# Performance work log

Hardware: AMD Instinct MI355X
Metric: run time of the kernel (lower is better)

Reference implementation:

```python
import jax, jax.numpy as jnp
import numpy as np

IN_FEATURES = 4096
OUT_FEATURES = 4096
BATCH, SEQ = 4, 2048

def setup_inputs() -> dict:
    key = jax.random.key(0)
    k1, k2, k3, k4, k5 = jax.random.split(key, 5)
    x = jax.random.normal(k1, (BATCH, SEQ, IN_FEATURES), dtype=jnp.float32)
    # int8 codes stored as int32 in [0, 255] (asymmetric uint8-style quantization)
    qweight = jax.random.randint(k2, (OUT_FEATURES, IN_FEATURES), 0, 255, dtype=jnp.int32)
    scales = jax.random.uniform(k3, (OUT_FEATURES,), dtype=jnp.float32) * 0.01 + 1e-3
    zero_points = jax.random.uniform(k4, (OUT_FEATURES,), dtype=jnp.float32) * 255.0
    bias = jax.random.normal(k5, (OUT_FEATURES,), dtype=jnp.float32)
    return {"x": x, "qweight": qweight, "scales": scales, "zero_points": zero_points, "bias": bias}

def reference(x, qweight, scales, zero_points, bias):
    # Per-output-channel dequantization: W[o, i] = (q[o, i] - zp[o]) * scale[o]
    w = (qweight.astype(jnp.float32) - zero_points[:, None]) * scales[:, None]  # [O, I]
    # y = x @ W.T + b, fused dequant + GEMM in the original ipex op
    y = jnp.einsum("bsi,oi->bso", x, w) + bias
    return y
```

## Files before the change

### kernel.cpp

```cpp
#include <hip/hip_runtime.h>
#include <hip/hip_bf16.h>

typedef __attribute__((ext_vector_type(4))) int i32x4;
typedef __attribute__((ext_vector_type(16))) int i32x16;

#define M_DIM 8192
#define N_DIM 4096
#define K_DIM 4096
#define BM 256
#define BN 256
#define BK 128
#define NT2 (K_DIM / BK)

static __device__ inline void gload_lds16(const void* g, void* l) {
  __builtin_amdgcn_global_load_lds(
      (const __attribute__((address_space(1))) unsigned int*)g,
      (__attribute__((address_space(3))) unsigned int*)l,
      16, 0, 0);
}

__global__ __launch_bounds__(256) void prep_x_i8(
    const float* __restrict__ x, char* __restrict__ xq,
    float* __restrict__ rx, float* __restrict__ sxf) {
  const int row = blockIdx.x;
  const int tid = threadIdx.x;
  const float4* xr = (const float4*)(x + (long)row * K_DIM);
  float4 v[4];
  float mx = 0.f;
#pragma unroll
  for (int i = 0; i < 4; ++i) {
    v[i] = xr[i * 256 + tid];
    mx = fmaxf(mx, fmaxf(fmaxf(fabsf(v[i].x), fabsf(v[i].y)),
                         fmaxf(fabsf(v[i].z), fabsf(v[i].w))));
  }
#pragma unroll
  for (int off = 32; off > 0; off >>= 1) mx = fmaxf(mx, __shfl_down(mx, off, 64));
  __shared__ float redm[4];
  __shared__ int reds[4];
  const int lane = tid & 63, w = tid >> 6;
  if (lane == 0) redm[w] = mx;
  __syncthreads();
  const float maxv = fmaxf(fmaxf(redm[0], redm[1]), fmaxf(redm[2], redm[3]));
  const float inv = maxv > 0.f ? 127.f / maxv : 0.f;
  int* xo = (int*)(xq + (long)row * K_DIM);
  int ssum = 0;
#pragma unroll
  for (int i = 0; i < 4; ++i) {
    const int q0 = __float2int_rn(v[i].x * inv);
    const int q1 = __float2int_rn(v[i].y * inv);
    const int q2 = __float2int_rn(v[i].z * inv);
    const int q3 = __float2int_rn(v[i].w * inv);
    ssum += q0 + q1 + q2 + q3;
    xo[i * 256 + tid] =
        (q0 & 255) | ((q1 & 255) << 8) | ((q2 & 255) << 16) | ((q3 & 255) << 24);
  }
#pragma unroll
  for (int off = 32; off > 0; off >>= 1) ssum += __shfl_down(ssum, off, 64);
  if (lane == 0) reds[w] = ssum;
  __syncthreads();
  if (tid == 0) {
    rx[row] = maxv * (1.f / 127.f);
    sxf[row] = (float)(reds[0] + reds[1] + reds[2] + reds[3]);
  }
}

__global__ __launch_bounds__(256) void prep_q_i8(
    const int* __restrict__ q, char* __restrict__ qb) {
  const long idx = (long)blockIdx.x * blockDim.x + threadIdx.x;
  const int4 v = ((const int4*)q)[idx];
  const int a = v.x - 128, b = v.y - 128, c = v.z - 128, d = v.w - 128;
  ((int*)qb)[idx] = (a & 255) | ((b & 255) << 8) | ((c & 255) << 16) | ((d & 255) << 24);
}

__global__ __launch_bounds__(512, 2) void wq_gemm_i8(
    const char* __restrict__ A,
    const char* __restrict__ B,
    const float* __restrict__ rx,
    const float* __restrict__ sxf,
    const float* __restrict__ scales,
    const float* __restrict__ zps,
    const float* __restrict__ bias,
    float* __restrict__ C) {
  __shared__ __align__(16) char lds[2 * 65536];

  const int tid = threadIdx.x;
  const int lane = tid & 63;
  const int wv = tid >> 6;
  const int wr = wv >> 2, wc = wv & 3;

  const int wg = blockIdx.x;
  const int lid = (wg & 7) * 64 + (wg >> 3);
  const int bx = lid & 15, by = lid >> 4;
  const int brow = by * BM;
  const int bcol = bx * BN;

  i32x16 acc[4][2] = {};

  const int srow = tid >> 3;
  const int schunk = ((tid & 7) ^ (srow & 7)) * 16;
  const int wub = (tid & ~63) * 16;
  const char* gAs = A + (long)(brow + srow) * K_DIM + schunk;
  const char* gBs = B + (long)(bcol + srow) * K_DIM + schunk;

#define STAGE_A2(T, J0, J1)                                                   \
  do {                                                                        \
    char* d = lds + ((T) & 1) * 65536;                                        \
    gload_lds16(gAs + (long)(J0) * 262144 + (long)(T) * 128,                  \
                d + (J0) * 8192 + wub);                                       \
    gload_lds16(gAs + (long)(J1) * 262144 + (long)(T) * 128,                  \
                d + (J1) * 8192 + wub);                                       \
  } while (0)
#define STAGE_B2(T, J0, J1)                                                   \
  do {                                                                        \
    char* d = lds + ((T) & 1) * 65536 + 32768;                                \
    gload_lds16(gBs + (long)(J0) * 262144 + (long)(T) * 128,                  \
                d + (J0) * 8192 + wub);                                       \
    gload_lds16(gBs + (long)(J1) * 262144 + (long)(T) * 128,                  \
                d + (J1) * 8192 + wub);                                       \
  } while (0)

  const int row5 = lane & 31;
  const int kg = lane >> 5;
  int aoff[4], boff[4];
#pragma unroll
  for (int ks = 0; ks < 4; ++ks) {
    const int ch = ((ks * 2 + kg) ^ (row5 & 7)) * 16;
    aoff[ks] = (wr * 128 + row5) * 128 + ch;
    boff[ks] = (wc * 64 + row5) * 128 + ch;
  }

#define RD_A(BB, FM, KS) (*(const i32x4*)(lds + (BB) + aoff[KS] + (FM) * 4096))
#define RD_B(BB, FN, KS) (*(const i32x4*)(lds + (BB) + 32768 + boff[KS] + (FN) * 4096))
#define MMA(FM, FN, AV, BV)                                                   \
  acc[FM][FN] = __builtin_amdgcn_mfma_i32_32x32x32_i8(AV, BV, acc[FM][FN], 0, 0, 0)

#define BAR() __builtin_amdgcn_s_barrier()
#define VMC(N)                                                                \
  do {                                                                        \
    asm volatile("s_waitcnt vmcnt(" #N ")");                                  \
    __builtin_amdgcn_sched_barrier(0);                                        \
  } while (0)

  STAGE_A2(0, 0, 2);
  STAGE_B2(0, 0, 2);
  STAGE_B2(0, 1, 3);
  STAGE_A2(0, 1, 3);
  VMC(2);
  BAR();

  i32x4 a00, a01, a10, a11, a20, a21, a30, a31;
  i32x4 b00, b10, b01, b11, b02, b12, b03, b13;

  for (int t = 0; t < NT2 - 1; ++t) {
    const int bb = (t & 1) * 65536;
    const int t1 = t + 1;
    a00 = RD_A(bb, 0, 0); a10 = RD_A(bb, 1, 0);
    a01 = RD_A(bb, 0, 1); a11 = RD_A(bb, 1, 1);
    a20 = RD_A(bb, 0, 2); a30 = RD_A(bb, 1, 2);
    a21 = RD_A(bb, 0, 3); a31 = RD_A(bb, 1, 3);
    b00 = RD_B(bb, 0, 0); b10 = RD_B(bb, 1, 0);
    b01 = RD_B(bb, 0, 1); b11 = RD_B(bb, 1, 1);
    b02 = RD_B(bb, 0, 2); b12 = RD_B(bb, 1, 2);
    b03 = RD_B(bb, 0, 3); b13 = RD_B(bb, 1, 3);
    STAGE_A2(t1, 0, 2);
    STAGE_B2(t1, 0, 2);
    STAGE_B2(t1, 1, 3);
    __builtin_amdgcn_s_setprio(1);
    MMA(0, 0, a00, b00); MMA(0, 1, a00, b10);
    MMA(1, 0, a10, b00); MMA(1, 1, a10, b10);
    MMA(0, 0, a01, b01); MMA(0, 1, a01, b11);
    MMA(1, 0, a11, b01); MMA(1, 1, a11, b11);
    MMA(0, 0, a20, b02); MMA(0, 1, a20, b12);
    MMA(1, 0, a30, b02); MMA(1, 1, a30, b12);
    MMA(0, 0, a21, b03); MMA(0, 1, a21, b13);
    MMA(1, 0, a31, b03); MMA(1, 1, a31, b13);
    __builtin_amdgcn_s_setprio(0);
    VMC(6);
    BAR();
    a00 = RD_A(bb, 2, 0); a10 = RD_A(bb, 3, 0);
    a01 = RD_A(bb, 2, 1); a11 = RD_A(bb, 3, 1);
    a20 = RD_A(bb, 2, 2); a30 = RD_A(bb, 3, 2);
    a21 = RD_A(bb, 2, 3); a31 = RD_A(bb, 3, 3);
    STAGE_A2(t1, 1, 3);
    __builtin_amdgcn_s_setprio(1);
    MMA(2, 0, a00, b00); MMA(2, 1, a00, b10);
    MMA(3, 0, a10, b00); MMA(3, 1, a10, b10);
    MMA(2, 0, a01, b01); MMA(2, 1, a01, b11);
    MMA(3, 0, a11, b01); MMA(3, 1, a11, b11);
    MMA(2, 0, a20, b02); MMA(2, 1, a20, b12);
    MMA(3, 0, a30, b02); MMA(3, 1, a30, b12);
    MMA(2, 0, a21, b03); MMA(2, 1, a21, b13);
    MMA(3, 0, a31, b03); MMA(3, 1, a31, b13);
    __builtin_amdgcn_s_setprio(0);
    VMC(2);
    BAR();
  }

  {
    const int bb = 65536;
    a00 = RD_A(bb, 0, 0); a10 = RD_A(bb, 1, 0);
    a01 = RD_A(bb, 0, 1); a11 = RD_A(bb, 1, 1);
    a20 = RD_A(bb, 0, 2); a30 = RD_A(bb, 1, 2);
    a21 = RD_A(bb, 0, 3); a31 = RD_A(bb, 1, 3);
    b00 = RD_B(bb, 0, 0); b10 = RD_B(bb, 1, 0);
    b01 = RD_B(bb, 0, 1); b11 = RD_B(bb, 1, 1);
    b02 = RD_B(bb, 0, 2); b12 = RD_B(bb, 1, 2);
    b03 = RD_B(bb, 0, 3); b13 = RD_B(bb, 1, 3);
    MMA(0, 0, a00, b00); MMA(0, 1, a00, b10);
    MMA(1, 0, a10, b00); MMA(1, 1, a10, b10);
    MMA(0, 0, a01, b01); MMA(0, 1, a01, b11);
    MMA(1, 0, a11, b01); MMA(1, 1, a11, b11);
    MMA(0, 0, a20, b02); MMA(0, 1, a20, b12);
    MMA(1, 0, a30, b02); MMA(1, 1, a30, b12);
    MMA(0, 0, a21, b03); MMA(0, 1, a21, b13);
    MMA(1, 0, a31, b03); MMA(1, 1, a31, b13);
    VMC(0);
    BAR();
    a00 = RD_A(bb, 2, 0); a10 = RD_A(bb, 3, 0);
    a01 = RD_A(bb, 2, 1); a11 = RD_A(bb, 3, 1);
    a20 = RD_A(bb, 2, 2); a30 = RD_A(bb, 3, 2);
    a21 = RD_A(bb, 2, 3); a31 = RD_A(bb, 3, 3);
    MMA(2, 0, a00, b00); MMA(2, 1, a00, b10);
    MMA(3, 0, a10, b00); MMA(3, 1, a10, b10);
    MMA(2, 0, a01, b01); MMA(2, 1, a01, b11);
    MMA(3, 0, a11, b01); MMA(3, 1, a11, b11);
    MMA(2, 0, a20, b02); MMA(2, 1, a20, b12);
    MMA(3, 0, a30, b02); MMA(3, 1, a30, b12);
    MMA(2, 0, a21, b03); MMA(2, 1, a21, b13);
    MMA(3, 0, a31, b03); MMA(3, 1, a31, b13);
  }

  float sc[2], zp[2], bs[2];
  int coln[2];
#pragma unroll
  for (int fn = 0; fn < 2; ++fn) {
    coln[fn] = bcol + wc * 64 + fn * 32 + row5;
    sc[fn] = scales[coln[fn]];
    zp[fn] = 128.f - zps[coln[fn]];
    bs[fn] = bias[coln[fn]];
  }
#pragma unroll
  for (int fm = 0; fm < 4; ++fm) {
#pragma unroll
    for (int r = 0; r < 16; ++r) {
      const int grow = brow + wr * 128 + fm * 32 + (r & 3) + 8 * (r >> 2) + 4 * kg;
      const float rxv = rx[grow];
      const float sxv = sxf[grow];
#pragma unroll
      for (int fn = 0; fn < 2; ++fn) {
        C[(long)grow * N_DIM + coln[fn]] =
            sc[fn] * rxv * ((float)acc[fm][fn][r] + zp[fn] * sxv) + bs[fn];
      }
    }
  }
}

extern "C" void kernel_launch(void* const* d_in, const int* in_sizes, int n_in,
                              void* d_out, int out_size, void* d_ws, size_t ws_size,
                              hipStream_t stream) {
  const float* x = (const float*)d_in[0];
  const int* qw = (const int*)d_in[1];
  const float* scales = (const float*)d_in[2];
  const float* zps = (const float*)d_in[3];
  const float* bias = (const float*)d_in[4];
  float* out = (float*)d_out;

  char* ws = (char*)d_ws;
  char* xq = ws;
  char* qb = ws + (size_t)32 * 1024 * 1024;
  float* rx = (float*)(ws + (size_t)48 * 1024 * 1024);
  float* sxf = (float*)(ws + (size_t)48 * 1024 * 1024 + 65536);

  hipLaunchKernelGGL(prep_x_i8, dim3(M_DIM), dim3(256), 0, stream, x, xq, rx, sxf);
  hipLaunchKernelGGL(prep_q_i8, dim3((N_DIM * K_DIM / 4) / 256), dim3(256), 0, stream,
                     qw, qb);
  hipLaunchKernelGGL(wq_gemm_i8, dim3((M_DIM / BM) * (N_DIM / BN)), dim3(512), 0,
                     stream, xq, qb, rx, sxf, scales, zps, bias, out);
}
```

Measured before the change: 192.7 us.

## Software-pipeline LDS fragment reads across k-tiles with register double buffering

Restructures the int8 MFMA main loop so that A and B fragments for the next half-step or next k-tile are read from LDS while the current MFMAs run. All global-to-LDS stages for tile t+1 are issued at the start of each iteration, and explicit lgkmcnt waits and sched barriers keep the reads and MFMAs in a fixed order. B offsets are now derived from the A offsets plus one constant, which frees registers. The cost is more live vector registers (three fragment sets) and a changed barrier placement that must still protect the double-buffered LDS from being overwritten early.

```diff
diff --git a/kernel.cpp b/kernel.cpp
--- a/kernel.cpp
+++ b/kernel.cpp
@@ -121,16 +121,16 @@
 
   const int row5 = lane & 31;
   const int kg = lane >> 5;
-  int aoff[4], boff[4];
+  int aoff[4];
 #pragma unroll
   for (int ks = 0; ks < 4; ++ks) {
     const int ch = ((ks * 2 + kg) ^ (row5 & 7)) * 16;
     aoff[ks] = (wr * 128 + row5) * 128 + ch;
-    boff[ks] = (wc * 64 + row5) * 128 + ch;
-  }
+  }
+  const int bdiff = (wc * 64 - wr * 128) * 128 + 32768;
 
 #define RD_A(BB, FM, KS) (*(const i32x4*)(lds + (BB) + aoff[KS] + (FM) * 4096))
-#define RD_B(BB, FN, KS) (*(const i32x4*)(lds + (BB) + 32768 + boff[KS] + (FN) * 4096))
+#define RD_B(BB, FN, KS) (*(const i32x4*)(lds + (BB) + aoff[KS] + bdiff + (FN) * 4096))
 #define MMA(FM, FN, AV, BV)                                                   \
   acc[FM][FN] = __builtin_amdgcn_mfma_i32_32x32x32_i8(AV, BV, acc[FM][FN], 0, 0, 0)
 
@@ -140,6 +140,16 @@
     asm volatile("s_waitcnt vmcnt(" #N ")");                                  \
     __builtin_amdgcn_sched_barrier(0);                                        \
   } while (0)
+#define LGK0()                                                                \
+  do {                                                                        \
+    asm volatile("s_waitcnt lgkmcnt(0)");                                     \
+    __builtin_amdgcn_sched_barrier(0);                                        \
+  } while (0)
+#define SCHED() __builtin_amdgcn_sched_barrier(0)
+
+  i32x4 fa00, fa01, fa02, fa03, fa10, fa11, fa12, fa13;
+  i32x4 ga00, ga01, ga02, ga03, ga10, ga11, ga12, ga13;
+  i32x4 vb00, vb01, vb02, vb03, vb10, vb11, vb12, vb13;
 
   STAGE_A2(0, 0, 2);
   STAGE_B2(0, 0, 2);
@@ -147,87 +157,77 @@
   STAGE_A2(0, 1, 3);
   VMC(2);
   BAR();
-
-  i32x4 a00, a01, a10, a11, a20, a21, a30, a31;
-  i32x4 b00, b10, b01, b11, b02, b12, b03, b13;
+  fa00 = RD_A(0, 0, 0); fa01 = RD_A(0, 0, 1); fa02 = RD_A(0, 0, 2); fa03 = RD_A(0, 0, 3);
+  fa10 = RD_A(0, 1, 0); fa11 = RD_A(0, 1, 1); fa12 = RD_A(0, 1, 2); fa13 = RD_A(0, 1, 3);
+  vb00 = RD_B(0, 0, 0); vb01 = RD_B(0, 0, 1); vb02 = RD_B(0, 0, 2); vb03 = RD_B(0, 0, 3);
+  vb10 = RD_B(0, 1, 0); vb11 = RD_B(0, 1, 1); vb12 = RD_B(0, 1, 2); vb13 = RD_B(0, 1, 3);
 
   for (int t = 0; t < NT2 - 1; ++t) {
     const int bb = (t & 1) * 65536;
+    const int nb = bb ^ 65536;
     const int t1 = t + 1;
-    a00 = RD_A(bb, 0, 0); a10 = RD_A(bb, 1, 0);
-    a01 = RD_A(bb, 0, 1); a11 = RD_A(bb, 1, 1);
-    a20 = RD_A(bb, 0, 2); a30 = RD_A(bb, 1, 2);
-    a21 = RD_A(bb, 0, 3); a31 = RD_A(bb, 1, 3);
-    b00 = RD_B(bb, 0, 0); b10 = RD_B(bb, 1, 0);
-    b01 = RD_B(bb, 0, 1); b11 = RD_B(bb, 1, 1);
-    b02 = RD_B(bb, 0, 2); b12 = RD_B(bb, 1, 2);
-    b03 = RD_B(bb, 0, 3); b13 = RD_B(bb, 1, 3);
     STAGE_A2(t1, 0, 2);
     STAGE_B2(t1, 0, 2);
     STAGE_B2(t1, 1, 3);
+    STAGE_A2(t1, 1, 3);
+    VMC(8);
+    BAR();
+    ga00 = RD_A(bb, 2, 0); ga01 = RD_A(bb, 2, 1); ga02 = RD_A(bb, 2, 2); ga03 = RD_A(bb, 2, 3);
+    ga10 = RD_A(bb, 3, 0); ga11 = RD_A(bb, 3, 1); ga12 = RD_A(bb, 3, 2); ga13 = RD_A(bb, 3, 3);
+    SCHED();
     __builtin_amdgcn_s_setprio(1);
-    MMA(0, 0, a00, b00); MMA(0, 1, a00, b10);
-    MMA(1, 0, a10, b00); MMA(1, 1, a10, b10);
-    MMA(0, 0, a01, b01); MMA(0, 1, a01, b11);
-    MMA(1, 0, a11, b01); MMA(1, 1, a11, b11);
-    MMA(0, 0, a20, b02); MMA(0, 1, a20, b12);
-    MMA(1, 0, a30, b02); MMA(1, 1, a30, b12);
-    MMA(0, 0, a21, b03); MMA(0, 1, a21, b13);
-    MMA(1, 0, a31, b03); MMA(1, 1, a31, b13);
+    MMA(0, 0, fa00, vb00); MMA(0, 1, fa00, vb10);
+    MMA(1, 0, fa10, vb00); MMA(1, 1, fa10, vb10);
+    MMA(0, 0, fa01, vb01); MMA(0, 1, fa01, vb11);
+    MMA(1, 0, fa11, vb01); MMA(1, 1, fa11, vb11);
+    MMA(0, 0, fa02, vb02); MMA(0, 1, fa02, vb12);
+    MMA(1, 0, fa12, vb02); MMA(1, 1, fa12, vb12);
+    MMA(0, 0, fa03, vb03); MMA(0, 1, fa03, vb13);
+    MMA(1, 0, fa13, vb03); MMA(1, 1, fa13, vb13);
     __builtin_amdgcn_s_setprio(0);
-    VMC(6);
-    BAR();
-    a00 = RD_A(bb, 2, 0); a10 = RD_A(bb, 3, 0);
-    a01 = RD_A(bb, 2, 1); a11 = RD_A(bb, 3, 1);
-    a20 = RD_A(bb, 2, 2); a30 = RD_A(bb, 3, 2);
-    a21 = RD_A(bb, 2, 3); a31 = RD_A(bb, 3, 3);
-    STAGE_A2(t1, 1, 3);
-    __builtin_amdgcn_s_setprio(1);
-    MMA(2, 0, a00, b00); MMA(2, 1, a00, b10);
-    MMA(3, 0, a10, b00); MMA(3, 1, a10, b10);
-    MMA(2, 0, a01, b01); MMA(2, 1, a01, b11);
-    MMA(3, 0, a11, b01); MMA(3, 1, a11, b11);
-    MMA(2, 0, a20, b02); MMA(2, 1, a20, b12);
-    MMA(3, 0, a30, b02); MMA(3, 1, a30, b12);
-    MMA(2, 0, a21, b03); MMA(2, 1, a21, b13);
-    MMA(3, 0, a31, b03); MMA(3, 1, a31, b13);
-    __builtin_amdgcn_s_setprio(0);
+    LGK0();
     VMC(2);
     BAR();
+    fa00 = RD_A(nb, 0, 0); fa01 = RD_A(nb, 0, 1); fa02 = RD_A(nb, 0, 2); fa03 = RD_A(nb, 0, 3);
+    fa10 = RD_A(nb, 1, 0); fa11 = RD_A(nb, 1, 1); fa12 = RD_A(nb, 1, 2); fa13 = RD_A(nb, 1, 3);
+    SCHED();
+    __builtin_amdgcn_s_setprio(1);
+    MMA(2, 0, ga00, vb00); MMA(2, 1, ga00, vb10);
+    MMA(3, 0, ga10, vb00); MMA(3, 1, ga10, vb10);
+    MMA(2, 0, ga01, vb01); MMA(2, 1, ga01, vb11);
+    MMA(3, 0, ga11, vb01); MMA(3, 1, ga11, vb11);
+    MMA(2, 0, ga02, vb02); MMA(2, 1, ga02, vb12);
+    MMA(3, 0, ga12, vb02); MMA(3, 1, ga12, vb12);
+    MMA(2, 0, ga03, vb03); MMA(2, 1, ga03, vb13);
+    MMA(3, 0, ga13, vb03); MMA(3, 1, ga13, vb13);
+    __builtin_amdgcn_s_setprio(0);
+    vb00 = RD_B(nb, 0, 0); vb01 = RD_B(nb, 0, 1); vb02 = RD_B(nb, 0, 2); vb03 = RD_B(nb, 0, 3);
+    vb10 = RD_B(nb, 1, 0); vb11 = RD_B(nb, 1, 1); vb12 = RD_B(nb, 1, 2); vb13 = RD_B(nb, 1, 3);
   }
 
   {
     const int bb = 65536;
-    a00 = RD_A(bb, 0, 0); a10 = RD_A(bb, 1, 0);
-    a01 = RD_A(bb, 0, 1); a11 = RD_A(bb, 1, 1);
-    a20 = RD_A(bb, 0, 2); a30 = RD_A(bb, 1, 2);
-    a21 = RD_A(bb, 0, 3); a31 = RD_A(bb, 1, 3);
-    b00 = RD_B(bb, 0, 0); b10 = RD_B(bb, 1, 0);
-    b01 = RD_B(bb, 0, 1); b11 = RD_B(bb, 1, 1);
-    b02 = RD_B(bb, 0, 2); b12 = RD_B(bb, 1, 2);
-    b03 = RD_B(bb, 0, 3); b13 = RD_B(bb, 1, 3);
-    MMA(0, 0, a00, b00); MMA(0, 1, a00, b10);
-    MMA(1, 0, a10, b00); MMA(1, 1, a10, b10);
-    MMA(0, 0, a01, b01); MMA(0, 1, a01, b11);
-    MMA(1, 0, a11, b01); MMA(1, 1, a11, b11);
-    MMA(0, 0, a20, b02); MMA(0, 1, a20, b12);
-    MMA(1, 0, a30, b02); MMA(1, 1, a30, b12);
-    MMA(0, 0, a21, b03); MMA(0, 1, a21, b13);
-    MMA(1, 0, a31, b03); MMA(1, 1, a31, b13);
     VMC(0);
     BAR();
-    a00 = RD_A(bb, 2, 0); a10 = RD_A(bb, 3, 0);
-    a01 = RD_A(bb, 2, 1); a11 = RD_A(bb, 3, 1);
-    a20 = RD_A(bb, 2, 2); a30 = RD_A(bb, 3, 2);
-    a21 = RD_A(bb, 2, 3); a31 = RD_A(bb, 3, 3);
-    MMA(2, 0, a00, b00); MMA(2, 1, a00, b10);
-    MMA(3, 0, a10, b00); MMA(3, 1, a10, b10);
-    MMA(2, 0, a01, b01); MMA(2, 1, a01, b11);
-    MMA(3, 0, a11, b01); MMA(3, 1, a11, b11);
-    MMA(2, 0, a20, b02); MMA(2, 1, a20, b12);
-    MMA(3, 0, a30, b02); MMA(3, 1, a30, b12);
-    MMA(2, 0, a21, b03); MMA(2, 1, a21, b13);
-    MMA(3, 0, a31, b03); MMA(3, 1, a31, b13);
+    ga00 = RD_A(bb, 2, 0); ga01 = RD_A(bb, 2, 1); ga02 = RD_A(bb, 2, 2); ga03 = RD_A(bb, 2, 3);
+    ga10 = RD_A(bb, 3, 0); ga11 = RD_A(bb, 3, 1); ga12 = RD_A(bb, 3, 2); ga13 = RD_A(bb, 3, 3);
+    SCHED();
+    MMA(0, 0, fa00, vb00); MMA(0, 1, fa00, vb10);
+    MMA(1, 0, fa10, vb00); MMA(1, 1, fa10, vb10);
+    MMA(0, 0, fa01, vb01); MMA(0, 1, fa01, vb11);
+    MMA(1, 0, fa11, vb01); MMA(1, 1, fa11, vb11);
+    MMA(0, 0, fa02, vb02); MMA(0, 1, fa02, vb12);
+    MMA(1, 0, fa12, vb02); MMA(1, 1, fa12, vb12);
+    MMA(0, 0, fa03, vb03); MMA(0, 1, fa03, vb13);
+    MMA(1, 0, fa13, vb03); MMA(1, 1, fa13, vb13);
+    MMA(2, 0, ga00, vb00); MMA(2, 1, ga00, vb10);
+    MMA(3, 0, ga10, vb00); MMA(3, 1, ga10, vb10);
+    MMA(2, 0, ga01, vb01); MMA(2, 1, ga01, vb11);
+    MMA(3, 0, ga11, vb01); MMA(3, 1, ga11, vb11);
+    MMA(2, 0, ga02, vb02); MMA(2, 1, ga02, vb12);
+    MMA(3, 0, ga12, vb02); MMA(3, 1, ga12, vb12);
+    MMA(2, 0, ga03, vb03); MMA(2, 1, ga03, vb13);
+    MMA(3, 0, ga13, vb03); MMA(3, 1, ga13, vb13);
   }
 
   float sc[2], zp[2], bs[2];
```

New measurement: 194.8 us. Within noise of the previous version (+1.1%).
